# Optimization experiments

Measured on AMD Instinct MI355X. Metric: run time of the kernel, lower is better.

Reference implementation:

```python
import jax, jax.numpy as jnp
import numpy as np

N = 100000
E = 1600000
NODE_DIM = 8
HIDDEN = 32
N_ACTIONS = 3


def _glorot(key, shape):
    fan_in, fan_out = shape[0], shape[1]
    lim = (6.0 / (fan_in + fan_out)) ** 0.5
    return jax.random.uniform(key, shape, jnp.float32, -lim, lim)


def setup_inputs() -> dict:
    key = jax.random.key(0)
    ks = jax.random.split(key, 16)
    x = jax.random.normal(ks[0], (N, NODE_DIM), jnp.float32)
    edge_index = jax.random.randint(ks[1], (2, E), 0, N, jnp.int64)
    # SAGEConv params: lin_l (aggregated neighbors, with bias), lin_r (root, no bias)
    params = {}
    dims = [(NODE_DIM, HIDDEN), (HIDDEN, HIDDEN), (HIDDEN, HIDDEN)]
    for i, (din, dout) in enumerate(dims, start=1):
        params[f"Wl{i}"] = _glorot(ks[2 * i], (din, dout))
        params[f"bl{i}"] = jnp.zeros((dout,), jnp.float32)
        params[f"Wr{i}"] = _glorot(ks[2 * i + 1], (din, dout))
    # MLP head
    params["Wh1"] = _glorot(ks[10], (HIDDEN, HIDDEN))
    params["bh1"] = jnp.zeros((HIDDEN,), jnp.float32)
    params["Wh2"] = _glorot(ks[11], (HIDDEN, N_ACTIONS))
    params["bh2"] = jnp.zeros((N_ACTIONS,), jnp.float32)
    return {"x": x, "edge_index": edge_index, **params}


def _sage_conv(x, src, dst, Wl, bl, Wr):
    # mean-aggregate neighbor features at each target node
    msg_sum = jax.ops.segment_sum(x[src], dst, num_segments=N)  # [N, d]
    deg = jax.ops.segment_sum(jnp.ones((src.shape[0],), x.dtype), dst, num_segments=N)
    mean = msg_sum / jnp.maximum(deg, 1.0)[:, None]
    return mean @ Wl + bl + x @ Wr


def reference(x, edge_index, Wl1, bl1, Wr1, Wl2, bl2, Wr2, Wl3, bl3, Wr3, Wh1, bh1, Wh2, bh2):
    src, dst = edge_index[0], edge_index[1]
    h = jax.nn.relu(_sage_conv(x, src, dst, Wl1, bl1, Wr1))
    h = jax.nn.relu(_sage_conv(h, src, dst, Wl2, bl2, Wr2))
    h = jax.nn.relu(_sage_conv(h, src, dst, Wl3, bl3, Wr3))
    h = jax.nn.relu(h @ Wh1 + bh1)
    return h @ Wh2 + bh2  # [N, n_actions]
```

## Files before the change

kernel.cpp:

```cpp
#include <hip/hip_runtime.h>
#include <hip/hip_bf16.h>

#define NN 100000
#define NE 1600000
#define DIN 8
#define DH 32
#define NACT 3
#define BKN 128
#define NBKT 782
#define CAPB 3072
#define PA 128
#define ECA (NE / PA)
#define LG32 (NN / 32)

typedef __hip_bfloat16 bf;
typedef unsigned short u16;
typedef __attribute__((ext_vector_type(8))) short bf16x8;
typedef __attribute__((ext_vector_type(4))) float f32x4;

__device__ __forceinline__ float bflo(unsigned u) { return __uint_as_float(u << 16); }
__device__ __forceinline__ float bfhi(unsigned u) { return __uint_as_float(u & 0xffff0000u); }
__device__ __forceinline__ unsigned pk2(float lo, float hi) {
    union { bf b; unsigned short u; } cl, ch;
    cl.b = __float2bfloat16(lo); ch.b = __float2bfloat16(hi);
    return (unsigned)cl.u | ((unsigned)ch.u << 16);
}

__launch_bounds__(256)
__global__ void prep_weights(const float* __restrict__ Wl1, const float* __restrict__ Wr1,
                             const float* __restrict__ Wl2, const float* __restrict__ Wr2,
                             const float* __restrict__ Wl3, const float* __restrict__ Wr3,
                             const float* __restrict__ Wh1,
                             u16* __restrict__ B1t, u16* __restrict__ B2t,
                             u16* __restrict__ B3t, u16* __restrict__ Bh1t) {
    int tid = threadIdx.x;
    for (int idx = tid; idx < 1024; idx += 256) {
        int j = idx >> 5, k = idx & 31;
        float v = (k < 8) ? Wl1[k * DH + j] : ((k < 16) ? Wr1[(k - 8) * DH + j] : 0.0f);
        reinterpret_cast<bf*>(B1t)[j * 32 + k] = __float2bfloat16(v);
    }
    for (int idx = tid; idx < 2048; idx += 256) {
        int j = idx >> 6, k = idx & 63;
        float v = (k < 32) ? Wl2[k * DH + j] : Wr2[(k - 32) * DH + j];
        reinterpret_cast<bf*>(B2t)[j * 64 + k] = __float2bfloat16(v);
    }
    for (int idx = tid; idx < 2048; idx += 256) {
        int j = idx >> 6, k = idx & 63;
        float v = (k < 32) ? Wl3[k * DH + j] : Wr3[(k - 32) * DH + j];
        reinterpret_cast<bf*>(B3t)[j * 64 + k] = __float2bfloat16(v);
    }
    for (int idx = tid; idx < 1024; idx += 256) {
        int j = idx >> 5, k = idx & 31;
        reinterpret_cast<bf*>(Bh1t)[j * 32 + k] = __float2bfloat16(Wh1[k * DH + j]);
    }
}

__launch_bounds__(256)
__global__ void partition_edges(const int* __restrict__ src, const int* __restrict__ dst,
                                int* __restrict__ bucket_cnt, unsigned* __restrict__ ebuf) {
    __shared__ int lcnt[NBKT];
    __shared__ int lbase[NBKT];
    int tid = threadIdx.x;
    for (int r = tid; r < NBKT; r += 256) lcnt[r] = 0;
    __syncthreads();

    int e0 = blockIdx.x * ECA;
    for (int e = e0 + tid * 4; e < e0 + ECA; e += 1024) {
        int4 d4 = *reinterpret_cast<const int4*>(&dst[e]);
        atomicAdd(&lcnt[(unsigned)d4.x >> 7], 1);
        atomicAdd(&lcnt[(unsigned)d4.y >> 7], 1);
        atomicAdd(&lcnt[(unsigned)d4.z >> 7], 1);
        atomicAdd(&lcnt[(unsigned)d4.w >> 7], 1);
    }
    __syncthreads();
    for (int r = tid; r < NBKT; r += 256) {
        lbase[r] = atomicAdd(&bucket_cnt[r], lcnt[r]);
        lcnt[r] = 0;
    }
    __syncthreads();
    for (int e = e0 + tid * 4; e < e0 + ECA; e += 1024) {
        int4 d4 = *reinterpret_cast<const int4*>(&dst[e]);
        int4 s4 = *reinterpret_cast<const int4*>(&src[e]);
        int r, p;
        r = (unsigned)d4.x >> 7; p = lbase[r] + atomicAdd(&lcnt[r], 1);
        if (p < CAPB) ebuf[r * CAPB + p] = ((unsigned)s4.x << 7) | ((unsigned)d4.x & 127u);
        r = (unsigned)d4.y >> 7; p = lbase[r] + atomicAdd(&lcnt[r], 1);
        if (p < CAPB) ebuf[r * CAPB + p] = ((unsigned)s4.y << 7) | ((unsigned)d4.y & 127u);
        r = (unsigned)d4.z >> 7; p = lbase[r] + atomicAdd(&lcnt[r], 1);
        if (p < CAPB) ebuf[r * CAPB + p] = ((unsigned)s4.z << 7) | ((unsigned)d4.z & 127u);
        r = (unsigned)d4.w >> 7; p = lbase[r] + atomicAdd(&lcnt[r], 1);
        if (p < CAPB) ebuf[r * CAPB + p] = ((unsigned)s4.w << 7) | ((unsigned)d4.w & 127u);
    }
}

__launch_bounds__(256)
__global__ void scan_buckets(const int* __restrict__ bucket_cnt, int* __restrict__ bucket_base) {
    __shared__ int s[256];
    int tid = threadIdx.x;
    int i0 = tid * 4;
    int v0 = (i0 + 0 < NBKT) ? min(bucket_cnt[i0 + 0], CAPB) : 0;
    int v1 = (i0 + 1 < NBKT) ? min(bucket_cnt[i0 + 1], CAPB) : 0;
    int v2 = (i0 + 2 < NBKT) ? min(bucket_cnt[i0 + 2], CAPB) : 0;
    int v3 = (i0 + 3 < NBKT) ? min(bucket_cnt[i0 + 3], CAPB) : 0;
    s[tid] = v0 + v1 + v2 + v3;
    __syncthreads();
#pragma unroll
    for (int off = 1; off < 256; off <<= 1) {
        int t = (tid >= off) ? s[tid - off] : 0;
        __syncthreads();
        s[tid] += t;
        __syncthreads();
    }
    int prev = (tid > 0) ? s[tid - 1] : 0;
    if (i0 + 0 < NBKT) bucket_base[i0 + 0] = prev;
    if (i0 + 1 < NBKT) bucket_base[i0 + 1] = prev + v0;
    if (i0 + 2 < NBKT) bucket_base[i0 + 2] = prev + v0 + v1;
    if (i0 + 3 < NBKT) bucket_base[i0 + 3] = prev + v0 + v1 + v2;
}

__launch_bounds__(256)
__global__ void fill_fused(const int* __restrict__ bucket_cnt, const int* __restrict__ bucket_base,
                           const unsigned* __restrict__ ebuf,
                           int* __restrict__ degI, int* __restrict__ startP,
                           int* __restrict__ adj) {
    __shared__ unsigned sc[CAPB];
    __shared__ int cnt[BKN];
    __shared__ int lofs[BKN];
    __shared__ int cur[BKN];
    int tid = threadIdx.x;
    int r = blockIdx.x;
    int n = min(bucket_cnt[r], CAPB);
    if (tid < BKN) { cnt[tid] = 0; cur[tid] = 0; }
    __syncthreads();
    const unsigned* eb = ebuf + r * CAPB;
    for (int i = tid; i < n; i += 256) {
        unsigned v = eb[i];
        sc[i] = v;
        atomicAdd(&cnt[v & 127u], 1);
    }
    __syncthreads();
    if (tid < BKN) lofs[tid] = cnt[tid];
    __syncthreads();
#pragma unroll
    for (int off = 1; off < BKN; off <<= 1) {
        int t = 0;
        if (tid < BKN && tid >= off) t = lofs[tid - off];
        __syncthreads();
        if (tid < BKN) lofs[tid] += t;
        __syncthreads();
    }
    if (tid < BKN) lofs[tid] -= cnt[tid];
    __syncthreads();
    int gbase = bucket_base[r];
    int node = r * BKN + tid;
    if (tid < BKN && node < NN) {
        degI[node]   = cnt[tid];
        startP[node] = gbase + lofs[tid];
    }
    __syncthreads();
    for (int i = tid; i < n; i += 256) {
        unsigned v = sc[i];
        int d = v & 127u;
        int p = atomicAdd(&cur[d], 1);
        adj[gbase + lofs[d] + p] = (int)(v >> 7);
    }
}

__launch_bounds__(128)
__global__ void layer1_mfma(const float* __restrict__ x, const int* __restrict__ degI,
                            const int* __restrict__ start, const int* __restrict__ adj,
                            const u16* __restrict__ Bt, const float* __restrict__ blv,
                            bf* __restrict__ hout) {
    __shared__ __align__(16) short sA[32 * 72];
    int tid = threadIdx.x;
    int base = blockIdx.x * 32;

    {
        int row = tid >> 2, part = tid & 3;
        *reinterpret_cast<uint2*>(&sA[row * 72 + 16 + part * 4]) = make_uint2(0u, 0u);
    }

    int g = tid >> 5, t = tid & 31;
    int nb = t >> 1, q = t & 1;
    int nbase = base + g * 8;
    int dgv = 0, stv = 0;
    if (t < 8) { dgv = degI[nbase + t]; stv = start[nbase + t]; }

#pragma unroll 4
    for (int i = 0; i < 8; ++i) {
        int dg  = __shfl(dgv, i, 32);
        int row = __shfl(stv, i, 32);
        int node = nbase + i;
        int idxreg = (t < dg) ? adj[row + t] : 0;
        float4 xv;
        if (t == 2 || t == 3)
            xv = *reinterpret_cast<const float4*>(&x[node * DIN + (t - 2) * 4]);
        float a[4] = {0.f, 0.f, 0.f, 0.f};
        int lim = min(dg, 32);
        int nit = (lim + 15) >> 4;
        for (int j = 0; j < nit; ++j) {
            int k = nb + j * 16;
            int s = __shfl(idxreg, k, 32);
            float4 v = *reinterpret_cast<const float4*>(&x[s * DIN + q * 4]);
            if (k < lim) { a[0] += v.x; a[1] += v.y; a[2] += v.z; a[3] += v.w; }
        }
        for (int k = 32 + nb; k < dg; k += 16) {
            int s = adj[row + k];
            float4 v = *reinterpret_cast<const float4*>(&x[s * DIN + q * 4]);
            a[0] += v.x; a[1] += v.y; a[2] += v.z; a[3] += v.w;
        }
#pragma unroll
        for (int m = 0; m < 4; ++m) {
            a[m] += __shfl_xor(a[m], 2);
            a[m] += __shfl_xor(a[m], 4);
            a[m] += __shfl_xor(a[m], 8);
            a[m] += __shfl_xor(a[m], 16);
        }
        int nrow = g * 8 + i;
        if (t < 2) {
            float inv = 1.0f / fmaxf((float)dg, 1.0f);
            uint2 mm;
            mm.x = pk2(a[0] * inv, a[1] * inv);
            mm.y = pk2(a[2] * inv, a[3] * inv);
            *reinterpret_cast<uint2*>(&sA[nrow * 72 + t * 4]) = mm;
        } else if (t < 4) {
            uint2 xm;
            xm.x = pk2(xv.x, xv.y);
            xm.y = pk2(xv.z, xv.w);
            *reinterpret_cast<uint2*>(&sA[nrow * 72 + 8 + (t - 2) * 4]) = xm;
        }
    }
    __syncthreads();

    int wid = tid >> 6, lane = tid & 63;
    int r16 = lane & 15, k8 = (lane >> 4) * 8;
    bf16x8 av = *reinterpret_cast<const bf16x8*>(&sA[(wid * 16 + r16) * 72 + k8]);
    bf16x8 b0 = *reinterpret_cast<const bf16x8*>(&Bt[r16 * 32 + k8]);
    bf16x8 b1 = *reinterpret_cast<const bf16x8*>(&Bt[(16 + r16) * 32 + k8]);
    f32x4 acc0 = {0.f, 0.f, 0.f, 0.f}, acc1 = {0.f, 0.f, 0.f, 0.f};
    acc0 = __builtin_amdgcn_mfma_f32_16x16x32_bf16(av, b0, acc0, 0, 0, 0);
    acc1 = __builtin_amdgcn_mfma_f32_16x16x32_bf16(av, b1, acc1, 0, 0, 0);
    float bias0 = blv[r16], bias1 = blv[16 + r16];
    int rbase = base + wid * 16 + (lane >> 4) * 4;
#pragma unroll
    for (int reg = 0; reg < 4; ++reg) {
        int node = rbase + reg;
        hout[node * DH + r16]      = __float2bfloat16(fmaxf(acc0[reg] + bias0, 0.f));
        hout[node * DH + 16 + r16] = __float2bfloat16(fmaxf(acc1[reg] + bias1, 0.f));
    }
}

__device__ __forceinline__ void gather32(const bf* __restrict__ hin,
                                         const int* __restrict__ degI,
                                         const int* __restrict__ start,
                                         const int* __restrict__ adj,
                                         short* sA, int base, int tid) {
    int g = tid >> 5, t = tid & 31;
    int nb = t >> 2, q = t & 3;
    int nbase = base + g * 8;
    int dgv = 0, stv = 0;
    if (t < 8) { dgv = degI[nbase + t]; stv = start[nbase + t]; }

#pragma unroll 4
    for (int i = 0; i < 8; ++i) {
        int dg  = __shfl(dgv, i, 32);
        int row = __shfl(stv, i, 32);
        int node = nbase + i;
        int idxreg = (t < dg) ? adj[row + t] : 0;
        uint4 xru;
        if ((t & 28) == 4)
            xru = *reinterpret_cast<const uint4*>(&hin[node * DH + (t - 4) * 8]);
        float a[8] = {0.f, 0.f, 0.f, 0.f, 0.f, 0.f, 0.f, 0.f};
        int lim = min(dg, 32);
        int nit = (lim + 7) >> 3;
        for (int j = 0; j < nit; ++j) {
            int k = nb + j * 8;
            int s = __shfl(idxreg, k, 32);
            uint4 u = *reinterpret_cast<const uint4*>(&hin[s * DH + q * 8]);
            if (k < lim) {
                a[0] += bflo(u.x); a[1] += bfhi(u.x);
                a[2] += bflo(u.y); a[3] += bfhi(u.y);
                a[4] += bflo(u.z); a[5] += bfhi(u.z);
                a[6] += bflo(u.w); a[7] += bfhi(u.w);
            }
        }
        for (int k = 32 + nb; k < dg; k += 8) {
            int s = adj[row + k];
            uint4 u = *reinterpret_cast<const uint4*>(&hin[s * DH + q * 8]);
            a[0] += bflo(u.x); a[1] += bfhi(u.x);
            a[2] += bflo(u.y); a[3] += bfhi(u.y);
            a[4] += bflo(u.z); a[5] += bfhi(u.z);
            a[6] += bflo(u.w); a[7] += bfhi(u.w);
        }
#pragma unroll
        for (int m = 0; m < 8; ++m) {
            a[m] += __shfl_xor(a[m], 4);
            a[m] += __shfl_xor(a[m], 8);
            a[m] += __shfl_xor(a[m], 16);
        }
        int nrow = g * 8 + i;
        if (t < 4) {
            float inv = 1.0f / fmaxf((float)dg, 1.0f);
            uint4 mm;
            mm.x = pk2(a[0] * inv, a[1] * inv);
            mm.y = pk2(a[2] * inv, a[3] * inv);
            mm.z = pk2(a[4] * inv, a[5] * inv);
            mm.w = pk2(a[6] * inv, a[7] * inv);
            *reinterpret_cast<uint4*>(&sA[nrow * 72 + t * 8]) = mm;
        } else if (t < 8) {
            *reinterpret_cast<uint4*>(&sA[nrow * 72 + 32 + (t - 4) * 8]) = xru;
        }
    }
}

__launch_bounds__(128)
__global__ void layer2_mfma(const bf* __restrict__ hin, const int* __restrict__ degI,
                            const int* __restrict__ start, const int* __restrict__ adj,
                            const u16* __restrict__ Bt, const float* __restrict__ blv,
                            bf* __restrict__ hout) {
    __shared__ __align__(16) short sA[32 * 72];
    int tid = threadIdx.x;
    int base = blockIdx.x * 32;

    gather32(hin, degI, start, adj, sA, base, tid);
    __syncthreads();

    int wid = tid >> 6, lane = tid & 63;
    int r16 = lane & 15, k8 = (lane >> 4) * 8;
    const short* ap = &sA[(wid * 16 + r16) * 72];
    bf16x8 av0 = *reinterpret_cast<const bf16x8*>(&ap[k8]);
    bf16x8 av1 = *reinterpret_cast<const bf16x8*>(&ap[32 + k8]);
    const u16* b0p = &Bt[r16 * 64];
    const u16* b1p = &Bt[(16 + r16) * 64];
    bf16x8 b00 = *reinterpret_cast<const bf16x8*>(&b0p[k8]);
    bf16x8 b01 = *reinterpret_cast<const bf16x8*>(&b0p[32 + k8]);
    bf16x8 b10 = *reinterpret_cast<const bf16x8*>(&b1p[k8]);
    bf16x8 b11 = *reinterpret_cast<const bf16x8*>(&b1p[32 + k8]);
    f32x4 acc0 = {0.f, 0.f, 0.f, 0.f}, acc1 = {0.f, 0.f, 0.f, 0.f};
    acc0 = __builtin_amdgcn_mfma_f32_16x16x32_bf16(av0, b00, acc0, 0, 0, 0);
    acc0 = __builtin_amdgcn_mfma_f32_16x16x32_bf16(av1, b01, acc0, 0, 0, 0);
    acc1 = __builtin_amdgcn_mfma_f32_16x16x32_bf16(av0, b10, acc1, 0, 0, 0);
    acc1 = __builtin_amdgcn_mfma_f32_16x16x32_bf16(av1, b11, acc1, 0, 0, 0);
    float bias0 = blv[r16], bias1 = blv[16 + r16];
    int rbase = base + wid * 16 + (lane >> 4) * 4;
#pragma unroll
    for (int reg = 0; reg < 4; ++reg) {
        int node = rbase + reg;
        hout[node * DH + r16]      = __float2bfloat16(fmaxf(acc0[reg] + bias0, 0.f));
        hout[node * DH + 16 + r16] = __float2bfloat16(fmaxf(acc1[reg] + bias1, 0.f));
    }
}

__launch_bounds__(128)
__global__ void layer3_mfma(const bf* __restrict__ hin, const int* __restrict__ degI,
                            const int* __restrict__ start, const int* __restrict__ adj,
                            const u16* __restrict__ B3t, const float* __restrict__ bl3,
                            const u16* __restrict__ Bh1t, const float* __restrict__ bh1,
                            const float* __restrict__ Wh2, const float* __restrict__ bh2,
                            float* __restrict__ out) {
    __shared__ __align__(16) short sA[32 * 72];
    __shared__ float sW2[NACT * DH];
    int tid = threadIdx.x;
    int base = blockIdx.x * 32;

    if (tid < NACT * DH) {
        int a = tid >> 5, k = tid & 31;
        sW2[a * DH + k] = Wh2[k * NACT + a];
    }

    gather32(hin, degI, start, adj, sA, base, tid);
    __syncthreads();

    int wid = tid >> 6, lane = tid & 63;
    int r16 = lane & 15, k8 = (lane >> 4) * 8;
    int rloc = wid * 16 + (lane >> 4) * 4;

    f32x4 acc0 = {0.f, 0.f, 0.f, 0.f}, acc1 = {0.f, 0.f, 0.f, 0.f};
    {
        const short* ap = &sA[(wid * 16 + r16) * 72];
        bf16x8 av0 = *reinterpret_cast<const bf16x8*>(&ap[k8]);
        bf16x8 av1 = *reinterpret_cast<const bf16x8*>(&ap[32 + k8]);
        const u16* b0p = &B3t[r16 * 64];
        const u16* b1p = &B3t[(16 + r16) * 64];
        bf16x8 b00 = *reinterpret_cast<const bf16x8*>(&b0p[k8]);
        bf16x8 b01 = *reinterpret_cast<const bf16x8*>(&b0p[32 + k8]);
        bf16x8 b10 = *reinterpret_cast<const bf16x8*>(&b1p[k8]);
        bf16x8 b11 = *reinterpret_cast<const bf16x8*>(&b1p[32 + k8]);
        acc0 = __builtin_amdgcn_mfma_f32_16x16x32_bf16(av0, b00, acc0, 0, 0, 0);
        acc0 = __builtin_amdgcn_mfma_f32_16x16x32_bf16(av1, b01, acc0, 0, 0, 0);
        acc1 = __builtin_amdgcn_mfma_f32_16x16x32_bf16(av0, b10, acc1, 0, 0, 0);
        acc1 = __builtin_amdgcn_mfma_f32_16x16x32_bf16(av1, b11, acc1, 0, 0, 0);
    }
    __syncthreads();

    bf* h3b = reinterpret_cast<bf*>(sA);
    {
        float bias0 = bl3[r16], bias1 = bl3[16 + r16];
#pragma unroll
        for (int reg = 0; reg < 4; ++reg) {
            int rr = rloc + reg;
            h3b[rr * 40 + r16]      = __float2bfloat16(fmaxf(acc0[reg] + bias0, 0.f));
            h3b[rr * 40 + 16 + r16] = __float2bfloat16(fmaxf(acc1[reg] + bias1, 0.f));
        }
    }
    __syncthreads();

    f32x4 d0 = {0.f, 0.f, 0.f, 0.f}, d1 = {0.f, 0.f, 0.f, 0.f};
    {
        bf16x8 av = *reinterpret_cast<const bf16x8*>(&h3b[(wid * 16 + r16) * 40 + k8]);
        bf16x8 b0 = *reinterpret_cast<const bf16x8*>(&Bh1t[r16 * 32 + k8]);
        bf16x8 b1 = *reinterpret_cast<const bf16x8*>(&Bh1t[(16 + r16) * 32 + k8]);
        d0 = __builtin_amdgcn_mfma_f32_16x16x32_bf16(av, b0, d0, 0, 0, 0);
        d1 = __builtin_amdgcn_mfma_f32_16x16x32_bf16(av, b1, d1, 0, 0, 0);
    }
    __syncthreads();

    float* shm = reinterpret_cast<float*>(sA);
    {
        float hb0 = bh1[r16], hb1 = bh1[16 + r16];
#pragma unroll
        for (int reg = 0; reg < 4; ++reg) {
            int rr = rloc + reg;
            shm[rr * 36 + r16]      = fmaxf(d0[reg] + hb0, 0.f);
            shm[rr * 36 + 16 + r16] = fmaxf(d1[reg] + hb1, 0.f);
        }
    }
    __syncthreads();

    {
        int m = tid >> 2, a = tid & 3;
        if (a < NACT) {
            float o = bh2[a];
            const float* hp = &shm[m * 36];
            const float* wp = &sW2[a * DH];
#pragma unroll
            for (int k = 0; k < DH; k += 4) {
                f32x4 hv = *reinterpret_cast<const f32x4*>(&hp[k]);
                f32x4 wv = *reinterpret_cast<const f32x4*>(&wp[k]);
                o += hv.x * wv.x + hv.y * wv.y + hv.z * wv.z + hv.w * wv.w;
            }
            out[(base + m) * NACT + a] = o;
        }
    }
}

extern "C" void kernel_launch(void* const* d_in, const int* in_sizes, int n_in,
                              void* d_out, int out_size, void* d_ws, size_t ws_size,
                              hipStream_t stream) {
    const float* x   = (const float*)d_in[0];
    const int*   ei  = (const int*)d_in[1];
    const int*   src = ei;
    const int*   dst = ei + NE;
    const float* Wl1 = (const float*)d_in[2];
    const float* bl1 = (const float*)d_in[3];
    const float* Wr1 = (const float*)d_in[4];
    const float* Wl2 = (const float*)d_in[5];
    const float* bl2 = (const float*)d_in[6];
    const float* Wr2 = (const float*)d_in[7];
    const float* Wl3 = (const float*)d_in[8];
    const float* bl3 = (const float*)d_in[9];
    const float* Wr3 = (const float*)d_in[10];
    const float* Wh1 = (const float*)d_in[11];
    const float* bh1 = (const float*)d_in[12];
    const float* Wh2 = (const float*)d_in[13];
    const float* bh2 = (const float*)d_in[14];
    float* out = (float*)d_out;

    int* bucket      = (int*)d_ws;
    int* bucket_base = bucket + NBKT;
    int* degI        = bucket_base + NBKT;
    int* startP      = degI + NN;
    int* adj         = startP + NN;
    unsigned* ebuf   = (unsigned*)(adj + NE);
    u16* B1t         = (u16*)(ebuf + NBKT * CAPB);
    u16* B2t         = B1t + 1024;
    u16* B3t         = B2t + 2048;
    u16* Bh1t        = B3t + 2048;
    bf*  hA          = (bf*)(Bh1t + 1024);
    bf*  hB          = hA + DH * NN;

    hipMemsetAsync(bucket, 0, NBKT * sizeof(int), stream);

    prep_weights<<<1, 256, 0, stream>>>(Wl1, Wr1, Wl2, Wr2, Wl3, Wr3, Wh1,
                                        B1t, B2t, B3t, Bh1t);

    partition_edges<<<PA, 256, 0, stream>>>(src, dst, bucket, ebuf);
    scan_buckets<<<1, 256, 0, stream>>>(bucket, bucket_base);
    fill_fused<<<NBKT, 256, 0, stream>>>(bucket, bucket_base, ebuf, degI, startP, adj);

    layer1_mfma<<<LG32, 128, 0, stream>>>(x, degI, startP, adj, B1t, bl1, hA);
    layer2_mfma<<<LG32, 128, 0, stream>>>(hA, degI, startP, adj, B2t, bl2, hB);
    layer3_mfma<<<LG32, 128, 0, stream>>>(hB, degI, startP, adj, B3t, bl3,
                                          Bh1t, bh1, Wh2, bh2, out);
}
```

Before: 222.5 us.

## Fold bucket scan into fill kernel and batch adjacency index loads in gathers

Drops the single-block scan_buckets launch: each fill_fused block now computes its own bucket base by summing the counts of all earlier buckets with a shared-memory reduction. The gather loops in layer1 and the shared gather32 helper are fully unrolled, and all eight nodes' degrees, starts and first adjacency indices are loaded up front so those loads can overlap. Root-feature loads move out of the per-node loop into one coalesced load by all threads. The cost is redundant count reads in every fill block (up to 782 per block) and higher register pressure from the unrolled arrays.

```diff
diff --git a/kernel.cpp b/kernel.cpp
--- a/kernel.cpp
+++ b/kernel.cpp
@@ -94,32 +94,7 @@
 }
 
 __launch_bounds__(256)
-__global__ void scan_buckets(const int* __restrict__ bucket_cnt, int* __restrict__ bucket_base) {
-    __shared__ int s[256];
-    int tid = threadIdx.x;
-    int i0 = tid * 4;
-    int v0 = (i0 + 0 < NBKT) ? min(bucket_cnt[i0 + 0], CAPB) : 0;
-    int v1 = (i0 + 1 < NBKT) ? min(bucket_cnt[i0 + 1], CAPB) : 0;
-    int v2 = (i0 + 2 < NBKT) ? min(bucket_cnt[i0 + 2], CAPB) : 0;
-    int v3 = (i0 + 3 < NBKT) ? min(bucket_cnt[i0 + 3], CAPB) : 0;
-    s[tid] = v0 + v1 + v2 + v3;
-    __syncthreads();
-#pragma unroll
-    for (int off = 1; off < 256; off <<= 1) {
-        int t = (tid >= off) ? s[tid - off] : 0;
-        __syncthreads();
-        s[tid] += t;
-        __syncthreads();
-    }
-    int prev = (tid > 0) ? s[tid - 1] : 0;
-    if (i0 + 0 < NBKT) bucket_base[i0 + 0] = prev;
-    if (i0 + 1 < NBKT) bucket_base[i0 + 1] = prev + v0;
-    if (i0 + 2 < NBKT) bucket_base[i0 + 2] = prev + v0 + v1;
-    if (i0 + 3 < NBKT) bucket_base[i0 + 3] = prev + v0 + v1 + v2;
-}
-
-__launch_bounds__(256)
-__global__ void fill_fused(const int* __restrict__ bucket_cnt, const int* __restrict__ bucket_base,
+__global__ void fill_fused(const int* __restrict__ bucket_cnt,
                            const unsigned* __restrict__ ebuf,
                            int* __restrict__ degI, int* __restrict__ startP,
                            int* __restrict__ adj) {
@@ -127,11 +102,22 @@
     __shared__ int cnt[BKN];
     __shared__ int lofs[BKN];
     __shared__ int cur[BKN];
+    __shared__ int sred[256];
     int tid = threadIdx.x;
     int r = blockIdx.x;
+    int part = 0;
+    for (int b = tid; b < r; b += 256) part += min(bucket_cnt[b], CAPB);
+    sred[tid] = part;
+    if (tid < BKN) { cnt[tid] = 0; cur[tid] = 0; }
+    __syncthreads();
+#pragma unroll
+    for (int off = 128; off > 0; off >>= 1) {
+        if (tid < off) sred[tid] += sred[tid + off];
+        __syncthreads();
+    }
+    int gbase = sred[0];
+
     int n = min(bucket_cnt[r], CAPB);
-    if (tid < BKN) { cnt[tid] = 0; cur[tid] = 0; }
-    __syncthreads();
     const unsigned* eb = ebuf + r * CAPB;
     for (int i = tid; i < n; i += 256) {
         unsigned v = eb[i];
@@ -151,7 +137,6 @@
     }
     if (tid < BKN) lofs[tid] -= cnt[tid];
     __syncthreads();
-    int gbase = bucket_base[r];
     int node = r * BKN + tid;
     if (tid < BKN && node < NN) {
         degI[node]   = cnt[tid];
@@ -186,26 +171,37 @@
     int dgv = 0, stv = 0;
     if (t < 8) { dgv = degI[nbase + t]; stv = start[nbase + t]; }
 
-#pragma unroll 4
+    int dg[8], row[8], idxreg[8];
+#pragma unroll
     for (int i = 0; i < 8; ++i) {
-        int dg  = __shfl(dgv, i, 32);
-        int row = __shfl(stv, i, 32);
-        int node = nbase + i;
-        int idxreg = (t < dg) ? adj[row + t] : 0;
-        float4 xv;
-        if (t == 2 || t == 3)
-            xv = *reinterpret_cast<const float4*>(&x[node * DIN + (t - 2) * 4]);
+        dg[i]  = __shfl(dgv, i, 32);
+        row[i] = __shfl(stv, i, 32);
+    }
+#pragma unroll
+    for (int i = 0; i < 8; ++i)
+        idxreg[i] = (t < dg[i]) ? adj[row[i] + t] : 0;
+
+    if (t < 16) {
+        float4 xv = *reinterpret_cast<const float4*>(&x[(nbase + (t >> 1)) * DIN + (t & 1) * 4]);
+        uint2 xm;
+        xm.x = pk2(xv.x, xv.y);
+        xm.y = pk2(xv.z, xv.w);
+        *reinterpret_cast<uint2*>(&sA[(g * 8 + (t >> 1)) * 72 + 8 + (t & 1) * 4]) = xm;
+    }
+
+#pragma unroll
+    for (int i = 0; i < 8; ++i) {
         float a[4] = {0.f, 0.f, 0.f, 0.f};
-        int lim = min(dg, 32);
+        int lim = min(dg[i], 32);
         int nit = (lim + 15) >> 4;
         for (int j = 0; j < nit; ++j) {
             int k = nb + j * 16;
-            int s = __shfl(idxreg, k, 32);
+            int s = __shfl(idxreg[i], k, 32);
             float4 v = *reinterpret_cast<const float4*>(&x[s * DIN + q * 4]);
             if (k < lim) { a[0] += v.x; a[1] += v.y; a[2] += v.z; a[3] += v.w; }
         }
-        for (int k = 32 + nb; k < dg; k += 16) {
-            int s = adj[row + k];
+        for (int k = 32 + nb; k < dg[i]; k += 16) {
+            int s = adj[row[i] + k];
             float4 v = *reinterpret_cast<const float4*>(&x[s * DIN + q * 4]);
             a[0] += v.x; a[1] += v.y; a[2] += v.z; a[3] += v.w;
         }
@@ -216,18 +212,12 @@
             a[m] += __shfl_xor(a[m], 8);
             a[m] += __shfl_xor(a[m], 16);
         }
-        int nrow = g * 8 + i;
         if (t < 2) {
-            float inv = 1.0f / fmaxf((float)dg, 1.0f);
+            float inv = 1.0f / fmaxf((float)dg[i], 1.0f);
             uint2 mm;
             mm.x = pk2(a[0] * inv, a[1] * inv);
             mm.y = pk2(a[2] * inv, a[3] * inv);
-            *reinterpret_cast<uint2*>(&sA[nrow * 72 + t * 4]) = mm;
-        } else if (t < 4) {
-            uint2 xm;
-            xm.x = pk2(xv.x, xv.y);
-            xm.y = pk2(xv.z, xv.w);
-            *reinterpret_cast<uint2*>(&sA[nrow * 72 + 8 + (t - 2) * 4]) = xm;
+            *reinterpret_cast<uint2*>(&sA[(g * 8 + i) * 72 + t * 4]) = mm;
         }
     }
     __syncthreads();
@@ -261,21 +251,29 @@
     int dgv = 0, stv = 0;
     if (t < 8) { dgv = degI[nbase + t]; stv = start[nbase + t]; }
 
-#pragma unroll 4
+    int dg[8], row[8], idxreg[8];
+#pragma unroll
     for (int i = 0; i < 8; ++i) {
-        int dg  = __shfl(dgv, i, 32);
-        int row = __shfl(stv, i, 32);
-        int node = nbase + i;
-        int idxreg = (t < dg) ? adj[row + t] : 0;
-        uint4 xru;
-        if ((t & 28) == 4)
-            xru = *reinterpret_cast<const uint4*>(&hin[node * DH + (t - 4) * 8]);
+        dg[i]  = __shfl(dgv, i, 32);
+        row[i] = __shfl(stv, i, 32);
+    }
+#pragma unroll
+    for (int i = 0; i < 8; ++i)
+        idxreg[i] = (t < dg[i]) ? adj[row[i] + t] : 0;
+
+    {
+        uint4 xru = *reinterpret_cast<const uint4*>(&hin[(nbase + (t >> 2)) * DH + (t & 3) * 8]);
+        *reinterpret_cast<uint4*>(&sA[(g * 8 + (t >> 2)) * 72 + 32 + (t & 3) * 8]) = xru;
+    }
+
+#pragma unroll
+    for (int i = 0; i < 8; ++i) {
         float a[8] = {0.f, 0.f, 0.f, 0.f, 0.f, 0.f, 0.f, 0.f};
-        int lim = min(dg, 32);
+        int lim = min(dg[i], 32);
         int nit = (lim + 7) >> 3;
         for (int j = 0; j < nit; ++j) {
             int k = nb + j * 8;
-            int s = __shfl(idxreg, k, 32);
+            int s = __shfl(idxreg[i], k, 32);
             uint4 u = *reinterpret_cast<const uint4*>(&hin[s * DH + q * 8]);
             if (k < lim) {
                 a[0] += bflo(u.x); a[1] += bfhi(u.x);
@@ -284,8 +282,8 @@
                 a[6] += bflo(u.w); a[7] += bfhi(u.w);
             }
         }
-        for (int k = 32 + nb; k < dg; k += 8) {
-            int s = adj[row + k];
+        for (int k = 32 + nb; k < dg[i]; k += 8) {
+            int s = adj[row[i] + k];
             uint4 u = *reinterpret_cast<const uint4*>(&hin[s * DH + q * 8]);
             a[0] += bflo(u.x); a[1] += bfhi(u.x);
             a[2] += bflo(u.y); a[3] += bfhi(u.y);
@@ -298,17 +296,14 @@
             a[m] += __shfl_xor(a[m], 8);
             a[m] += __shfl_xor(a[m], 16);
         }
-        int nrow = g * 8 + i;
         if (t < 4) {
-            float inv = 1.0f / fmaxf((float)dg, 1.0f);
+            float inv = 1.0f / fmaxf((float)dg[i], 1.0f);
             uint4 mm;
             mm.x = pk2(a[0] * inv, a[1] * inv);
             mm.y = pk2(a[2] * inv, a[3] * inv);
             mm.z = pk2(a[4] * inv, a[5] * inv);
             mm.w = pk2(a[6] * inv, a[7] * inv);
-            *reinterpret_cast<uint4*>(&sA[nrow * 72 + t * 8]) = mm;
-        } else if (t < 8) {
-            *reinterpret_cast<uint4*>(&sA[nrow * 72 + 32 + (t - 4) * 8]) = xru;
+            *reinterpret_cast<uint4*>(&sA[(g * 8 + i) * 72 + t * 8]) = mm;
         }
     }
 }
@@ -467,8 +462,7 @@
     float* out = (float*)d_out;
 
     int* bucket      = (int*)d_ws;
-    int* bucket_base = bucket + NBKT;
-    int* degI        = bucket_base + NBKT;
+    int* degI        = bucket + NBKT;
     int* startP      = degI + NN;
     int* adj         = startP + NN;
     unsigned* ebuf   = (unsigned*)(adj + NE);
@@ -485,8 +479,7 @@
                                         B1t, B2t, B3t, Bh1t);
 
     partition_edges<<<PA, 256, 0, stream>>>(src, dst, bucket, ebuf);
-    scan_buckets<<<1, 256, 0, stream>>>(bucket, bucket_base);
-    fill_fused<<<NBKT, 256, 0, stream>>>(bucket, bucket_base, ebuf, degI, startP, adj);
+    fill_fused<<<NBKT, 256, 0, stream>>>(bucket, ebuf, degI, startP, adj);
 
     layer1_mfma<<<LG32, 128, 0, stream>>>(x, degI, startP, adj, B1t, bl1, hA);
     layer2_mfma<<<LG32, 128, 0, stream>>>(hA, degI, startP, adj, B2t, bl2, hB);
```

Measured after the change: 216.6 us. -2.6%, faster.
